# Performance work log

Hardware: AMD Instinct MI355X
Metric: run time of the kernel (lower is better)

Reference implementation:

```python
import jax, jax.numpy as jnp
import numpy as np


def _conv1x1(x, W, b):
    # x: (n, c_in, h, w); W: (c_out, c_in); b: (c_out,)
    return jnp.einsum('nchw,oc->nohw', x, W) + b[None, :, None, None]


def setup_inputs() -> dict:
    key = jax.random.key(0)
    ks = jax.random.split(key, 9)
    n, C, h, w = 2, 256, 64, 64
    Ch = C // 2
    s_in = 0.02
    return {
        'feature': jax.random.normal(ks[0], (n, C, h, w), dtype=jnp.float32),
        'Wq': jax.random.normal(ks[1], (Ch, C), dtype=jnp.float32) * s_in,
        'bq': jax.random.normal(ks[2], (Ch,), dtype=jnp.float32) * s_in,
        'Wk': jax.random.normal(ks[3], (Ch, C), dtype=jnp.float32) * s_in,
        'bk': jax.random.normal(ks[4], (Ch,), dtype=jnp.float32) * s_in,
        'Wv': jax.random.normal(ks[5], (Ch, C), dtype=jnp.float32) * s_in,
        'bv': jax.random.normal(ks[6], (Ch,), dtype=jnp.float32) * s_in,
        'Wm': jax.random.normal(ks[7], (C, Ch), dtype=jnp.float32) * s_in,
        'bm': jax.random.normal(ks[8], (C,), dtype=jnp.float32) * s_in,
    }


def reference(feature, Wq, bq, Wk, bk, Wv, bv, Wm, bm):
    n, C, h, w = feature.shape
    Ch = C // 2
    N = n * h * w
    # 1x1 conv projections, then flatten batch+spatial into one sequence dim
    q = _conv1x1(feature, Wq, bq)  # (n, Ch, h, w)
    k = _conv1x1(feature, Wk, bk)
    v = _conv1x1(feature, Wv, bv)
    # NCHW -> NHWC -> (N, Ch), matching torch transpose(1,2).transpose(2,3).reshape
    q = jnp.transpose(q, (0, 2, 3, 1)).reshape(N, Ch)
    k = jnp.transpose(k, (0, 2, 3, 1)).reshape(N, Ch)
    v = jnp.transpose(v, (0, 2, 3, 1)).reshape(N, Ch)
    # scores = k @ q.T (note: torch code uses k as rows, q.T as cols)
    scores = k @ q.T  # (N, N)
    attn = jax.nn.softmax(scores, axis=-1)
    mask = attn @ v  # (N, Ch)
    mask = mask.reshape(n, h, w, Ch)
    # torch transpose chain (2,3)->(1,2)->(2,3): (n,h,w,Ch) -> (n,Ch,w,h)
    mask = jnp.transpose(mask, (0, 3, 2, 1))
    out = _conv1x1(mask, Wm, bm)  # (n, C, w, h); h==w so residual add is valid
    return out + feature
```

## Files before the change

### kernel.cpp

```cpp
#include <hip/hip_runtime.h>
#include <hip/hip_bf16.h>

#define LOG2E 1.44269504088896340736f

typedef __attribute__((ext_vector_type(8))) short short8;
typedef __attribute__((ext_vector_type(4))) float f32x4;
typedef __attribute__((ext_vector_type(2))) unsigned int uint2v;
typedef __attribute__((ext_vector_type(4))) unsigned int uint4v;
typedef unsigned int u32;

__device__ __forceinline__ short f2bf(float f) {
    unsigned u = __builtin_bit_cast(unsigned, f);
    unsigned r = (u + 0x7FFFu + ((u >> 16) & 1u)) >> 16;
    return (short)r;
}

__device__ __forceinline__ float bf2f(short x) {
    unsigned u = ((unsigned)(unsigned short)x) << 16;
    return __builtin_bit_cast(float, u);
}

__device__ __forceinline__ unsigned cvt_pk_bf16(float lo, float hi) {
    unsigned r;
    asm volatile("v_cvt_pk_bf16_f32 %0, %1, %2" : "=v"(r) : "v"(lo), "v"(hi));
    return r;
}

__device__ __forceinline__ float fexp2(float x) {
    float r;
    asm("v_exp_f32 %0, %1" : "=v"(r) : "v"(x));
    return r;
}

__global__ __launch_bounds__(64) void wprep_kernel(
    const float* __restrict__ Wq, const float* __restrict__ bq,
    const float* __restrict__ Wk, const float* __restrict__ bk,
    const float* __restrict__ Wv, const float* __restrict__ bv,
    const float* __restrict__ Wm,
    short* __restrict__ Wb, float* __restrict__ bqkv, short* __restrict__ Wmb)
{
    const int b = blockIdx.x;
    const int t = threadIdx.x;
    if (b < 384) {
        const int mat = b >> 7, row = b & 127;
        const float* src = (mat == 0 ? Wq : mat == 1 ? Wk : Wv) + (size_t)row * 256;
        const float sc = (mat == 1) ? LOG2E : 1.f;
        float4 v = *(const float4*)(src + t * 4);
        uint2v pk;
        pk.x = cvt_pk_bf16(v.x * sc, v.y * sc);
        pk.y = cvt_pk_bf16(v.z * sc, v.w * sc);
        *(uint2v*)(Wb + (size_t)b * 256 + t * 4) = pk;
    } else if (b == 384) {
        for (int e = t; e < 384; e += 64) {
            const int mat = e >> 7;
            const float* bsrc = (mat == 0 ? bq : mat == 1 ? bk : bv);
            bqkv[e] = bsrc[e & 127] * (mat == 1 ? LOG2E : 1.f);
        }
    } else {
        const int row = b - 385;
        float2 v = *(const float2*)(Wm + (size_t)row * 128 + t * 2);
        *(u32*)(Wmb + (size_t)row * 128 + t * 2) = cvt_pk_bf16(v.x, v.y);
    }
}

__global__ __launch_bounds__(256) void proj_kernel(
    const float* __restrict__ feat, const short* __restrict__ Wb,
    const float* __restrict__ bqkv,
    short* __restrict__ Qb, short* __restrict__ Kb, short* __restrict__ VTp)
{
    __shared__ __align__(16) short Xs[16 * 256];
    __shared__ __align__(16) short VTs[128 * 16];
    const int t = threadIdx.x;
    const int blk = blockIdx.x;
    const int ib = blk * 16;
    const int n = ib >> 12;
    const int hw0 = ib & 4095;

    {
        const int r = t & 15, cg = t >> 4;
        const float* fp = feat + (size_t)n * 1048576 + (size_t)(cg * 16) * 4096 + hw0 + r;
        short8 t0, t1;
        #pragma unroll
        for (int ci = 0; ci < 8; ++ci) {
            t0[ci] = f2bf(fp[(size_t)ci * 4096]);
            t1[ci] = f2bf(fp[(size_t)(ci + 8) * 4096]);
        }
        const int sw = (r & 7) << 2;
        *(short8*)(&Xs[r * 256 + ((cg * 2) ^ sw) * 8]) = t0;
        *(short8*)(&Xs[r * 256 + ((cg * 2 + 1) ^ sw) * 8]) = t1;
    }
    __syncthreads();

    const int lane = t & 63;
    const int w = __builtin_amdgcn_readfirstlane(t >> 6);
    const int l15 = lane & 15;
    const int g = lane >> 4;
    const int o0w = w * 96;

    f32x4 acc[6];
    #pragma unroll
    for (int osub = 0; osub < 6; ++osub)
        acc[osub] = *(const f32x4*)(bqkv + o0w + osub * 16 + 4 * g);

    const short* wbase = Wb + (size_t)(o0w + l15) * 256 + g * 8;
    const int xsw = (l15 & 7) << 2;
    #pragma unroll
    for (int kc = 0; kc < 8; ++kc) {
        short8 xf = *(const short8*)(&Xs[l15 * 256 + (((kc * 4 + g) ^ xsw) * 8)]);
        #pragma unroll
        for (int osub = 0; osub < 6; ++osub) {
            short8 wf = *(const short8*)(wbase + (size_t)osub * 16 * 256 + kc * 32);
            acc[osub] = __builtin_amdgcn_mfma_f32_16x16x32_bf16(wf, xf, acc[osub], 0, 0, 0);
        }
    }

    #pragma unroll
    for (int osub = 0; osub < 6; ++osub) {
        const int o0 = o0w + osub * 16;
        const int mat = o0 >> 7;
        const int col = (o0 & 127) + 4 * g;
        if (mat == 0) {
            uint2v pk;
            pk.x = cvt_pk_bf16(acc[osub][0], acc[osub][1]);
            pk.y = cvt_pk_bf16(acc[osub][2], acc[osub][3]);
            *(uint2v*)(Qb + (size_t)(ib + l15) * 128 + col) = pk;
        } else if (mat == 1) {
            uint2v pk;
            pk.x = cvt_pk_bf16(acc[osub][0], acc[osub][1]);
            pk.y = cvt_pk_bf16(acc[osub][2], acc[osub][3]);
            *(uint2v*)(Kb + (size_t)(ib + l15) * 128 + col) = pk;
        } else {
            #pragma unroll
            for (int reg = 0; reg < 4; ++reg)
                VTs[(col + reg) * 16 + l15] = f2bf(acc[osub][reg]);
        }
    }
    __syncthreads();

    {
        const int o = t >> 1, ih = (t & 1) * 8;
        short8 vv = *(const short8*)(&VTs[o * 16 + ih]);
        const int base32 = ib & ~31;
        const int u = (ib >> 4) & 1;
        const int p0 = 2 * ih + 4 * u;
        uint4v q = __builtin_bit_cast(uint4v, vv);
        uint2v lo; lo.x = q.x; lo.y = q.y;
        uint2v hi; hi.x = q.z; hi.y = q.w;
        *(uint2v*)(VTp + (size_t)o * 8192 + base32 + p0) = lo;
        *(uint2v*)(VTp + (size_t)o * 8192 + base32 + p0 + 8) = hi;
    }
}

__global__ __launch_bounds__(256, 2) void attn_kernel(
    const short* __restrict__ Qb, const short* __restrict__ Kb,
    const short* __restrict__ VTp,
    short* __restrict__ Opart, float* __restrict__ Ssb)
{
    __shared__ __align__(16) char smem[65536];

    const int tid = threadIdx.x;
    const int lane = tid & 63;
    const int w = __builtin_amdgcn_readfirstlane(tid >> 6);
    const int l15 = lane & 15;
    const int g = lane >> 4;
    const int blk = blockIdx.x;
    const int ibX = blk >> 4;
    const int jq  = blk & 15;
    const int iw  = ibX * 128 + w * 32;
    const int j0  = jq * 512;

    short8 kf[2][4];
    #pragma unroll
    for (int iset = 0; iset < 2; ++iset)
        #pragma unroll
        for (int dcq = 0; dcq < 4; ++dcq)
            kf[iset][dcq] = *(const short8*)(Kb + (size_t)(iw + iset * 16 + l15) * 128 + dcq * 32 + g * 8);

    f32x4 O[2][8];
    #pragma unroll
    for (int iset = 0; iset < 2; ++iset)
        #pragma unroll
        for (int dc = 0; dc < 8; ++dc) O[iset][dc] = (f32x4){0.f, 0.f, 0.f, 0.f};
    float s[2] = {0.f, 0.f};

    const short* srcQ0;
    const short* srcQ1;
    const short* srcV0;
    const short* srcV1;
    {
        int r0 = 4 * w + (lane >> 4), c0 = lane & 15;
        srcQ0 = Qb + (size_t)(j0 + r0) * 128 + (c0 ^ (r0 & 7)) * 8;
        int r1 = 16 + 4 * w + (lane >> 4);
        srcQ1 = Qb + (size_t)(j0 + r1) * 128 + (c0 ^ (r1 & 7)) * 8;
        int d0 = 16 * w + (lane >> 2), c2 = lane & 3;
        srcV0 = VTp + (size_t)d0 * 8192 + j0 + (c2 ^ (d0 & 3)) * 8;
        int d1 = 64 + 16 * w + (lane >> 2);
        srcV1 = VTp + (size_t)d1 * 8192 + j0 + (c2 ^ (d1 & 3)) * 8;
    }

    auto stage = [&](int quarter) {
        char* base = smem + quarter * 16384;
        __builtin_amdgcn_global_load_lds(
            (const __attribute__((address_space(1))) u32*)(const void*)srcQ0,
            (__attribute__((address_space(3))) u32*)(void*)(base + w * 1024), 16, 0, 0);
        __builtin_amdgcn_global_load_lds(
            (const __attribute__((address_space(1))) u32*)(const void*)srcQ1,
            (__attribute__((address_space(3))) u32*)(void*)(base + (4 + w) * 1024), 16, 0, 0);
        __builtin_amdgcn_global_load_lds(
            (const __attribute__((address_space(1))) u32*)(const void*)srcV0,
            (__attribute__((address_space(3))) u32*)(void*)(base + (8 + w) * 1024), 16, 0, 0);
        __builtin_amdgcn_global_load_lds(
            (const __attribute__((address_space(1))) u32*)(const void*)srcV1,
            (__attribute__((address_space(3))) u32*)(void*)(base + (12 + w) * 1024), 16, 0, 0);
        srcQ0 += 32 * 128;
        srcQ1 += 32 * 128;
        srcV0 += 32;
        srcV1 += 32;
    };

    auto compute32 = [&](const char* base) {
        const char* Qt = base;
        const char* Vt = base + 8192;
        const int xs = (l15 & 7) << 4;

        f32x4 sv[2][2];
        #pragma unroll
        for (int jh = 0; jh < 2; ++jh)
            #pragma unroll
            for (int iset = 0; iset < 2; ++iset)
                sv[jh][iset] = (f32x4){-16.f, -16.f, -16.f, -16.f};

        __builtin_amdgcn_s_setprio(1);
        #pragma unroll
        for (int dcq = 0; dcq < 4; ++dcq) {
            short8 qa0 = *(const short8*)(Qt + ((l15 * 256 + dcq * 64 + g * 16) ^ xs));
            short8 qa1 = *(const short8*)(Qt + (((l15 + 16) * 256 + dcq * 64 + g * 16) ^ xs));
            sv[0][0] = __builtin_amdgcn_mfma_f32_16x16x32_bf16(qa0, kf[0][dcq], sv[0][0], 0, 0, 0);
            sv[0][1] = __builtin_amdgcn_mfma_f32_16x16x32_bf16(qa0, kf[1][dcq], sv[0][1], 0, 0, 0);
            sv[1][0] = __builtin_amdgcn_mfma_f32_16x16x32_bf16(qa1, kf[0][dcq], sv[1][0], 0, 0, 0);
            sv[1][1] = __builtin_amdgcn_mfma_f32_16x16x32_bf16(qa1, kf[1][dcq], sv[1][1], 0, 0, 0);
        }
        __builtin_amdgcn_s_setprio(0);

        short8 pf[2];
        #pragma unroll
        for (int iset = 0; iset < 2; ++iset) {
            float p0[4], p1[4], ps = 0.f;
            #pragma unroll
            for (int e = 0; e < 4; ++e) {
                p0[e] = fexp2(sv[0][iset][e]);
                p1[e] = fexp2(sv[1][iset][e]);
                ps += p0[e] + p1[e];
            }
            s[iset] += ps;
            uint4v pk;
            pk.x = cvt_pk_bf16(p0[0], p0[1]);
            pk.y = cvt_pk_bf16(p0[2], p0[3]);
            pk.z = cvt_pk_bf16(p1[0], p1[1]);
            pk.w = cvt_pk_bf16(p1[2], p1[3]);
            pf[iset] = __builtin_bit_cast(short8, pk);
        }

        __builtin_amdgcn_s_setprio(1);
        #pragma unroll
        for (int dc = 0; dc < 8; ++dc) {
            short8 va = *(const short8*)(Vt + (dc * 16 + l15) * 64 + ((g ^ (l15 & 3)) << 4));
            O[0][dc] = __builtin_amdgcn_mfma_f32_16x16x32_bf16(va, pf[0], O[0][dc], 0, 0, 0);
            O[1][dc] = __builtin_amdgcn_mfma_f32_16x16x32_bf16(va, pf[1], O[1][dc], 0, 0, 0);
        }
        __builtin_amdgcn_s_setprio(0);
    };

    stage(0);
    stage(1);
    __syncthreads();
    for (int tt = 0; tt < 16; tt += 2) {
        if (tt + 2 < 16) {
            stage((tt + 2) & 3);
            stage((tt + 3) & 3);
        }
        compute32(smem + (tt & 3) * 16384);
        compute32(smem + ((tt + 1) & 3) * 16384);
        __syncthreads();
    }

    #pragma unroll
    for (int iset = 0; iset < 2; ++iset) {
        const int i = iw + iset * 16 + l15;
        #pragma unroll
        for (int dc = 0; dc < 8; ++dc) {
            uint2v pk;
            pk.x = cvt_pk_bf16(O[iset][dc][0], O[iset][dc][1]);
            pk.y = cvt_pk_bf16(O[iset][dc][2], O[iset][dc][3]);
            *(uint2v*)(Opart + (size_t)(jq * 8192 + i) * 128 + dc * 16 + 4 * g) = pk;
        }
        Ssb[(((size_t)jq * 8192 + i) << 2) + g] = s[iset];
    }
}

__global__ __launch_bounds__(256) void merge_kernel(
    const short* __restrict__ Opart, const float* __restrict__ Ssb,
    short* __restrict__ maskbb)
{
    const int t = threadIdx.x, b = blockIdx.x;
    const int row = b * 32 + (t >> 3);
    const int d0 = (t & 7) * 16;

    float T = 0.f;
    #pragma unroll
    for (int q = 0; q < 16; ++q) {
        f32x4 s4 = *(const f32x4*)(Ssb + (((size_t)q * 8192 + row) << 2));
        T += (s4[0] + s4[1]) + (s4[2] + s4[3]);
    }

    float acc[16];
    #pragma unroll
    for (int e = 0; e < 16; ++e) acc[e] = 0.f;
    #pragma unroll
    for (int q = 0; q < 16; ++q) {
        const short* op = Opart + (size_t)(q * 8192 + row) * 128 + d0;
        short8 o0 = *(const short8*)(op);
        short8 o1 = *(const short8*)(op + 8);
        #pragma unroll
        for (int e = 0; e < 8; ++e) {
            acc[e]     += bf2f(o0[e]);
            acc[8 + e] += bf2f(o1[e]);
        }
    }
    const float inv = 1.f / T;
    uint4v pk0, pk1;
    pk0.x = cvt_pk_bf16(acc[0] * inv, acc[1] * inv);
    pk0.y = cvt_pk_bf16(acc[2] * inv, acc[3] * inv);
    pk0.z = cvt_pk_bf16(acc[4] * inv, acc[5] * inv);
    pk0.w = cvt_pk_bf16(acc[6] * inv, acc[7] * inv);
    pk1.x = cvt_pk_bf16(acc[8] * inv, acc[9] * inv);
    pk1.y = cvt_pk_bf16(acc[10] * inv, acc[11] * inv);
    pk1.z = cvt_pk_bf16(acc[12] * inv, acc[13] * inv);
    pk1.w = cvt_pk_bf16(acc[14] * inv, acc[15] * inv);
    short* mp = maskbb + (size_t)row * 128 + d0;
    *(uint4v*)(mp) = pk0;
    *(uint4v*)(mp + 8) = pk1;
}

__global__ __launch_bounds__(256, 4) void epi_kernel(
    const short* __restrict__ maskbb, const short* __restrict__ Wmb,
    const float* __restrict__ bm, const float* __restrict__ feat,
    float* __restrict__ out)
{
    __shared__ __align__(16) short Ms[16 * 128];
    const int t = threadIdx.x;
    const int blk = blockIdx.x;
    const int yt = blk & 3;
    const int x = (blk >> 2) & 63;
    const int n = blk >> 8;
    const int y0 = yt * 16;

    {
        const int r = t >> 4, c = t & 15;
        const int i = n * 4096 + (y0 + r) * 64 + x;
        short8 v = *(const short8*)(maskbb + (size_t)i * 128 + c * 8);
        *(short8*)(&Ms[r * 128 + ((c ^ ((r & 7) << 1)) * 8)]) = v;
    }
    __syncthreads();

    const int lane = t & 63;
    const int w = __builtin_amdgcn_readfirstlane(t >> 6);
    const int l15 = lane & 15;
    const int g = lane >> 4;
    const int c0 = w * 64;

    short8 bf[4];
    const int msw = (l15 & 7) << 1;
    #pragma unroll
    for (int dcq = 0; dcq < 4; ++dcq)
        bf[dcq] = *(const short8*)(&Ms[l15 * 128 + (((dcq * 4 + g) ^ msw) * 8)]);

    f32x4 acc[4];
    #pragma unroll
    for (int ct = 0; ct < 4; ++ct)
        acc[ct] = *(const f32x4*)(bm + c0 + ct * 16 + 4 * g);

    const short* wbase = Wmb + (size_t)(c0 + l15) * 128 + g * 8;
    #pragma unroll
    for (int dcq = 0; dcq < 4; ++dcq) {
        #pragma unroll
        for (int ct = 0; ct < 4; ++ct) {
            short8 wf = *(const short8*)(wbase + (size_t)ct * 16 * 128 + dcq * 32);
            acc[ct] = __builtin_amdgcn_mfma_f32_16x16x32_bf16(wf, bf[dcq], acc[ct], 0, 0, 0);
        }
    }

    #pragma unroll
    for (int ct = 0; ct < 4; ++ct) {
        #pragma unroll
        for (int reg = 0; reg < 4; ++reg) {
            const int c = c0 + ct * 16 + 4 * g + reg;
            const size_t oidx = (((size_t)(n * 256 + c) * 64 + x) * 64) + y0 + l15;
            out[oidx] = acc[ct][reg] + feat[oidx];
        }
    }
}

extern "C" void kernel_launch(void* const* d_in, const int* in_sizes, int n_in,
                              void* d_out, int out_size, void* d_ws, size_t ws_size,
                              hipStream_t stream) {
    const float* feat = (const float*)d_in[0];
    const float* Wq = (const float*)d_in[1];
    const float* bq = (const float*)d_in[2];
    const float* Wk = (const float*)d_in[3];
    const float* bk = (const float*)d_in[4];
    const float* Wv = (const float*)d_in[5];
    const float* bv = (const float*)d_in[6];
    const float* Wm = (const float*)d_in[7];
    const float* bm = (const float*)d_in[8];
    float* out = (float*)d_out;

    short* Qb = (short*)d_ws;
    short* Kb = Qb + 8192 * 128;
    short* VTp = Kb + 8192 * 128;
    short* maskbb = VTp + 8192 * 128;
    short* Opart = maskbb + 8192 * 128;
    float* Ssb = (float*)(Opart + (size_t)16 * 8192 * 128);
    float* bqkv = Ssb + (size_t)16 * 8192 * 4;
    short* Wb = (short*)(bqkv + 384);
    short* Wmb = Wb + 384 * 256;

    hipLaunchKernelGGL(wprep_kernel, dim3(641), dim3(64), 0, stream,
                       Wq, bq, Wk, bk, Wv, bv, Wm, Wb, bqkv, Wmb);
    hipLaunchKernelGGL(proj_kernel, dim3(512), dim3(256), 0, stream,
                       feat, Wb, bqkv, Qb, Kb, VTp);
    hipLaunchKernelGGL(attn_kernel, dim3(1024), dim3(256), 0, stream,
                       Qb, Kb, VTp, Opart, Ssb);
    hipLaunchKernelGGL(merge_kernel, dim3(256), dim3(256), 0, stream,
                       Opart, Ssb, maskbb);
    hipLaunchKernelGGL(epi_kernel, dim3(512), dim3(256), 0, stream,
                       maskbb, Wmb, bm, feat, out);
}
```

Measured before the change: 81.48 us.

## Software-pipeline attention loop with vmcnt barriers and fuse merge into epilogue

The attention loop now runs as a one-stage skewed pipeline: each iteration does the PV MFMAs of the previous tile and the QK plus exp of the current tile. It replaces full __syncthreads with a partial s_waitcnt vmcnt(4) plus a barrier, so one staged tile's loads stay in flight across compute. The separate merge kernel is removed, and the epilogue sums the 16 partial outputs and partial softmax denominators directly into its LDS tile. This saves a launch and the maskbb round trip, but the epilogue now reads the partials itself and its loads become heavier.

```diff
diff --git a/kernel.cpp b/kernel.cpp
--- a/kernel.cpp
+++ b/kernel.cpp
@@ -31,6 +31,13 @@
     asm("v_exp_f32 %0, %1" : "=v"(r) : "v"(x));
     return r;
 }
+
+#define WAIT_BAR4 { asm volatile("s_waitcnt vmcnt(4)" ::: "memory"); \
+                    __builtin_amdgcn_s_barrier(); \
+                    __builtin_amdgcn_sched_barrier(0); }
+#define WAIT_BAR0 { asm volatile("s_waitcnt vmcnt(0)" ::: "memory"); \
+                    __builtin_amdgcn_s_barrier(); \
+                    __builtin_amdgcn_sched_barrier(0); }
 
 __global__ __launch_bounds__(64) void wprep_kernel(
     const float* __restrict__ Wq, const float* __restrict__ bq,
@@ -182,6 +189,7 @@
         #pragma unroll
         for (int dc = 0; dc < 8; ++dc) O[iset][dc] = (f32x4){0.f, 0.f, 0.f, 0.f};
     float s[2] = {0.f, 0.f};
+    short8 pf[2];
 
     const short* srcQ0;
     const short* srcQ1;
@@ -218,9 +226,8 @@
         srcV1 += 32;
     };
 
-    auto compute32 = [&](const char* base) {
+    auto QKSM = [&](const char* base) {
         const char* Qt = base;
-        const char* Vt = base + 8192;
         const int xs = (l15 & 7) << 4;
 
         f32x4 sv[2][2];
@@ -230,7 +237,6 @@
             for (int iset = 0; iset < 2; ++iset)
                 sv[jh][iset] = (f32x4){-16.f, -16.f, -16.f, -16.f};
 
-        __builtin_amdgcn_s_setprio(1);
         #pragma unroll
         for (int dcq = 0; dcq < 4; ++dcq) {
             short8 qa0 = *(const short8*)(Qt + ((l15 * 256 + dcq * 64 + g * 16) ^ xs));
@@ -240,9 +246,7 @@
             sv[1][0] = __builtin_amdgcn_mfma_f32_16x16x32_bf16(qa1, kf[0][dcq], sv[1][0], 0, 0, 0);
             sv[1][1] = __builtin_amdgcn_mfma_f32_16x16x32_bf16(qa1, kf[1][dcq], sv[1][1], 0, 0, 0);
         }
-        __builtin_amdgcn_s_setprio(0);
-
-        short8 pf[2];
+
         #pragma unroll
         for (int iset = 0; iset < 2; ++iset) {
             float p0[4], p1[4], ps = 0.f;
@@ -260,7 +264,11 @@
             pk.w = cvt_pk_bf16(p1[2], p1[3]);
             pf[iset] = __builtin_bit_cast(short8, pk);
         }
-
+    };
+
+    auto PV = [&](const char* base) {
+        const char* Vt = base + 8192;
+        const int xs = (l15 & 7) << 4;
         __builtin_amdgcn_s_setprio(1);
         #pragma unroll
         for (int dc = 0; dc < 8; ++dc) {
@@ -273,16 +281,22 @@
 
     stage(0);
     stage(1);
-    __syncthreads();
-    for (int tt = 0; tt < 16; tt += 2) {
-        if (tt + 2 < 16) {
-            stage((tt + 2) & 3);
-            stage((tt + 3) & 3);
-        }
-        compute32(smem + (tt & 3) * 16384);
-        compute32(smem + ((tt + 1) & 3) * 16384);
-        __syncthreads();
-    }
+    WAIT_BAR4;
+    stage(2);
+    QKSM(smem);
+    for (int tt = 1; tt <= 13; ++tt) {
+        WAIT_BAR4;
+        stage(tt + 2);
+        PV(smem + ((tt - 1) & 3) * 16384);
+        QKSM(smem + (tt & 3) * 16384);
+    }
+    WAIT_BAR4;
+    PV(smem + (13 & 3) * 16384);
+    QKSM(smem + (14 & 3) * 16384);
+    WAIT_BAR0;
+    PV(smem + (14 & 3) * 16384);
+    QKSM(smem + (15 & 3) * 16384);
+    PV(smem + (15 & 3) * 16384);
 
     #pragma unroll
     for (int iset = 0; iset < 2; ++iset) {
@@ -298,54 +312,10 @@
     }
 }
 
-__global__ __launch_bounds__(256) void merge_kernel(
+__global__ __launch_bounds__(256, 4) void epi_kernel(
     const short* __restrict__ Opart, const float* __restrict__ Ssb,
-    short* __restrict__ maskbb)
-{
-    const int t = threadIdx.x, b = blockIdx.x;
-    const int row = b * 32 + (t >> 3);
-    const int d0 = (t & 7) * 16;
-
-    float T = 0.f;
-    #pragma unroll
-    for (int q = 0; q < 16; ++q) {
-        f32x4 s4 = *(const f32x4*)(Ssb + (((size_t)q * 8192 + row) << 2));
-        T += (s4[0] + s4[1]) + (s4[2] + s4[3]);
-    }
-
-    float acc[16];
-    #pragma unroll
-    for (int e = 0; e < 16; ++e) acc[e] = 0.f;
-    #pragma unroll
-    for (int q = 0; q < 16; ++q) {
-        const short* op = Opart + (size_t)(q * 8192 + row) * 128 + d0;
-        short8 o0 = *(const short8*)(op);
-        short8 o1 = *(const short8*)(op + 8);
-        #pragma unroll
-        for (int e = 0; e < 8; ++e) {
-            acc[e]     += bf2f(o0[e]);
-            acc[8 + e] += bf2f(o1[e]);
-        }
-    }
-    const float inv = 1.f / T;
-    uint4v pk0, pk1;
-    pk0.x = cvt_pk_bf16(acc[0] * inv, acc[1] * inv);
-    pk0.y = cvt_pk_bf16(acc[2] * inv, acc[3] * inv);
-    pk0.z = cvt_pk_bf16(acc[4] * inv, acc[5] * inv);
-    pk0.w = cvt_pk_bf16(acc[6] * inv, acc[7] * inv);
-    pk1.x = cvt_pk_bf16(acc[8] * inv, acc[9] * inv);
-    pk1.y = cvt_pk_bf16(acc[10] * inv, acc[11] * inv);
-    pk1.z = cvt_pk_bf16(acc[12] * inv, acc[13] * inv);
-    pk1.w = cvt_pk_bf16(acc[14] * inv, acc[15] * inv);
-    short* mp = maskbb + (size_t)row * 128 + d0;
-    *(uint4v*)(mp) = pk0;
-    *(uint4v*)(mp + 8) = pk1;
-}
-
-__global__ __launch_bounds__(256, 4) void epi_kernel(
-    const short* __restrict__ maskbb, const short* __restrict__ Wmb,
-    const float* __restrict__ bm, const float* __restrict__ feat,
-    float* __restrict__ out)
+    const short* __restrict__ Wmb, const float* __restrict__ bm,
+    const float* __restrict__ feat, float* __restrict__ out)
 {
     __shared__ __align__(16) short Ms[16 * 128];
     const int t = threadIdx.x;
@@ -358,8 +328,27 @@
     {
         const int r = t >> 4, c = t & 15;
         const int i = n * 4096 + (y0 + r) * 64 + x;
-        short8 v = *(const short8*)(maskbb + (size_t)i * 128 + c * 8);
-        *(short8*)(&Ms[r * 128 + ((c ^ ((r & 7) << 1)) * 8)]) = v;
+        float acc8[8] = {0.f, 0.f, 0.f, 0.f, 0.f, 0.f, 0.f, 0.f};
+        #pragma unroll
+        for (int q = 0; q < 16; ++q) {
+            short8 o = *(const short8*)(Opart + ((size_t)q * 8192 + i) * 128 + c * 8);
+            #pragma unroll
+            for (int e = 0; e < 8; ++e) acc8[e] += bf2f(o[e]);
+        }
+        f32x4 s4 = *(const f32x4*)(Ssb + (((size_t)c * 8192 + i) << 2));
+        float tp = (s4[0] + s4[1]) + (s4[2] + s4[3]);
+        tp += __shfl_xor(tp, 1);
+        tp += __shfl_xor(tp, 2);
+        tp += __shfl_xor(tp, 4);
+        tp += __shfl_xor(tp, 8);
+        const float inv = 1.f / tp;
+        uint4v pk;
+        pk.x = cvt_pk_bf16(acc8[0] * inv, acc8[1] * inv);
+        pk.y = cvt_pk_bf16(acc8[2] * inv, acc8[3] * inv);
+        pk.z = cvt_pk_bf16(acc8[4] * inv, acc8[5] * inv);
+        pk.w = cvt_pk_bf16(acc8[6] * inv, acc8[7] * inv);
+        *(short8*)(&Ms[r * 128 + ((c ^ ((r & 7) << 1)) * 8)]) =
+            __builtin_bit_cast(short8, pk);
     }
     __syncthreads();
 
@@ -418,8 +407,7 @@
     short* Qb = (short*)d_ws;
     short* Kb = Qb + 8192 * 128;
     short* VTp = Kb + 8192 * 128;
-    short* maskbb = VTp + 8192 * 128;
-    short* Opart = maskbb + 8192 * 128;
+    short* Opart = VTp + 8192 * 128;
     float* Ssb = (float*)(Opart + (size_t)16 * 8192 * 128);
     float* bqkv = Ssb + (size_t)16 * 8192 * 4;
     short* Wb = (short*)(bqkv + 384);
@@ -431,8 +419,6 @@
                        feat, Wb, bqkv, Qb, Kb, VTp);
     hipLaunchKernelGGL(attn_kernel, dim3(1024), dim3(256), 0, stream,
                        Qb, Kb, VTp, Opart, Ssb);
-    hipLaunchKernelGGL(merge_kernel, dim3(256), dim3(256), 0, stream,
-                       Opart, Ssb, maskbb);
     hipLaunchKernelGGL(epi_kernel, dim3(512), dim3(256), 0, stream,
-                       maskbb, Wmb, bm, feat, out);
-}
+                       Opart, Ssb, Wmb, bm, feat, out);
+}
```

Measured after the change: 79.72 us. 2.2% less time.
